# Kernel tuning notes

Measured on AMD Instinct MI355X. Metric: run time of the kernel, lower is better.

Reference implementation:

```python
import jax, jax.numpy as jnp
import numpy as np


def setup_inputs() -> dict:
    key = jax.random.key(0)
    ks = jax.random.split(key, 9)
    b, h, w, c = 32, 64, 64, 256
    s = 0.02  # small init to mimic variance-scaled NIN weights
    return {
        "x": jax.random.normal(ks[0], (b, h, w, c), dtype=jnp.float32),
        "Wq": jax.random.normal(ks[1], (c, c), dtype=jnp.float32) * s,
        "bq": jnp.zeros((c,), dtype=jnp.float32),
        "Wk": jax.random.normal(ks[2], (c, c), dtype=jnp.float32) * s,
        "bk": jnp.zeros((c,), dtype=jnp.float32),
        "Wv": jax.random.normal(ks[3], (c, c), dtype=jnp.float32) * s,
        "bv": jnp.zeros((c,), dtype=jnp.float32),
        "Wo": jax.random.normal(ks[4], (c, c), dtype=jnp.float32) * s,
        "bo": jnp.zeros((c,), dtype=jnp.float32),
    }


def reference(x, Wq, bq, Wk, bk, Wv, bv, Wo, bo):
    # x: [b, h, w, c]. NOTE: in the source, GroupNorm(x) is computed but its
    # output is immediately overwritten (dead code); Q/K/V come from raw x.
    b, h, w, c = x.shape
    cf = jnp.asarray(c, x.dtype)
    Q = jnp.einsum('bhwc,cd->bhwd', x, Wq) + bq
    K = jnp.einsum('bhwc,cd->bhwd', x, Wk) + bk
    V = jnp.einsum('bhwc,cd->bhwd', x, Wv) + bv
    # per-row attention over the W axis: scores [b, h, w, w]
    # double scaling: /(c*sqrt(1/2)) then softmax(./sqrt(c))
    scores = jnp.einsum('bhic,bhjc->bhij', Q, K) / (cf * jnp.sqrt(jnp.asarray(0.5, x.dtype)))
    attn = jax.nn.softmax(scores / jnp.sqrt(cf), axis=-1)
    out = jnp.einsum('bhij,bhjc->bhic', attn, V)
    out = jnp.einsum('bhwc,cd->bhwd', out, Wo) + bo
    return out + x
```

## Files before the change

### kernel.cpp

```cpp
#include <hip/hip_runtime.h>
#include <hip/hip_bf16.h>
#include <stdint.h>


typedef __bf16 bf16x8 __attribute__((ext_vector_type(8)));
typedef __bf16 bf16x4 __attribute__((ext_vector_type(4)));
typedef float f32x4 __attribute__((ext_vector_type(4)));

#define C 256
#define WTOK 64
#define CP 264
#define VP 72
#define PP 72

__device__ float  g_wT[3 * 65536];
__device__ __bf16 g_wqk[65536];
__device__ __bf16 g_wvo[65536];
__device__ float  g_c[256];
__device__ float  g_bvo[256];

__device__ __forceinline__ bf16x8 ld8(const __bf16* p) {
  return *reinterpret_cast<const bf16x8*>(p);
}

__global__ __launch_bounds__(256) void trans_kernel(
    const float* __restrict__ wq, const float* __restrict__ wk,
    const float* __restrict__ wv) {
  __shared__ float tile[32][33];
  const float* src = (blockIdx.z == 0) ? wq : (blockIdx.z == 1) ? wk : wv;
  float* d = &g_wT[0] + (size_t)blockIdx.z * 65536;
  const int tx = threadIdx.x, ty = threadIdx.y;
  const int k0 = blockIdx.x * 32;
  const int m0 = blockIdx.y * 32;
  for (int i = 0; i < 4; ++i)
    tile[ty + 8 * i][tx] = src[(size_t)(k0 + ty + 8 * i) * 256 + m0 + tx];
  __syncthreads();
  for (int i = 0; i < 4; ++i)
    d[(size_t)(m0 + ty + 8 * i) * 256 + k0 + tx] = tile[tx][ty + 8 * i];
}

__global__ __launch_bounds__(256) void fold_kernel(
    const float* __restrict__ wk, const float* __restrict__ wo) {
  const int n = blockIdx.x;
  const int k = threadIdx.x;
  float acc = 0.f;
  if (blockIdx.y == 0) {
    const float* a = &g_wT[0];
    #pragma unroll 8
    for (int m = 0; m < 256; ++m) acc += a[m * 256 + k] * wk[n * 256 + m];
    g_wqk[n * 256 + k] = (__bf16)acc;
  } else {
    const float* a = &g_wT[2 * 65536];
    #pragma unroll 8
    for (int m = 0; m < 256; ++m) acc += a[m * 256 + k] * wo[m * 256 + n];
    g_wvo[n * 256 + k] = (__bf16)acc;
  }
}

__global__ __launch_bounds__(256) void bias_kernel(
    const float* __restrict__ bq, const float* __restrict__ bv,
    const float* __restrict__ bo, const float* __restrict__ wo) {
  const int n = threadIdx.x;
  const float* wkT = &g_wT[65536];
  float c = 0.f, bb = bo[n];
  #pragma unroll 8
  for (int m = 0; m < 256; ++m) c += bq[m] * wkT[m * 256 + n];
  #pragma unroll 8
  for (int k = 0; k < 256; ++k) bb += bv[k] * wo[k * 256 + n];
  g_c[n] = c;
  g_bvo[n] = bb;
}

__global__ __launch_bounds__(256, 2) void attn_fused_kernel(
    const float* __restrict__ x, float* __restrict__ out) {
  __shared__ __align__(16) __bf16 smem[39936];
  __bf16* xs = smem;
  __bf16* ts = smem + 16896;
  __bf16* vt = ts;
  __bf16* ps = smem + 35328;

  const int tid = threadIdx.x;
  const int wv = tid >> 6;
  const int lane = tid & 63;
  const int quad = lane >> 4;
  const int l16 = lane & 15;
  const int bh = blockIdx.x;
  const float* xrow = x + (size_t)bh * (WTOK * C);

  for (int it = 0; it < 16; ++it) {
    const int chunk = tid + it * 256;
    const int row = chunk >> 6;
    const int c4 = (chunk & 63) << 2;
    const float4 v = *reinterpret_cast<const float4*>(xrow + row * 256 + c4);
    bf16x4 b;
    b[0] = (__bf16)v.x; b[1] = (__bf16)v.y; b[2] = (__bf16)v.z; b[3] = (__bf16)v.w;
    *reinterpret_cast<bf16x4*>(xs + row * CP + c4) = b;
  }
  __syncthreads();

  const int nb = wv * 64;
  const int i0 = wv * 16;

  {
    f32x4 D[4][4];
    const f32x4 zero = {0.f, 0.f, 0.f, 0.f};
    for (int m = 0; m < 4; ++m)
      for (int nt = 0; nt < 4; ++nt) D[m][nt] = zero;
    for (int kc = 0; kc < 8; ++kc) {
      const int ko = kc * 32 + quad * 8;
      bf16x8 a[4];
      for (int m = 0; m < 4; ++m) a[m] = ld8(xs + (m * 16 + l16) * CP + ko);
      for (int nt = 0; nt < 4; ++nt) {
        bf16x8 b = ld8(g_wqk + (size_t)(nb + nt * 16 + l16) * 256 + ko);
        for (int m = 0; m < 4; ++m)
          D[m][nt] = __builtin_amdgcn_mfma_f32_16x16x32_bf16(a[m], b, D[m][nt], 0, 0, 0);
      }
    }
    float cs[4];
    for (int nt = 0; nt < 4; ++nt) cs[nt] = g_c[nb + nt * 16 + l16];
    for (int m = 0; m < 4; ++m)
      for (int nt = 0; nt < 4; ++nt)
        for (int r = 0; r < 4; ++r)
          ts[(m * 16 + quad * 4 + r) * CP + nb + nt * 16 + l16] =
              (__bf16)(D[m][nt][r] + cs[nt]);
  }
  __syncthreads();

  f32x4 S[4];
  {
    const f32x4 zero = {0.f, 0.f, 0.f, 0.f};
    for (int nt = 0; nt < 4; ++nt) S[nt] = zero;
    bf16x8 qa[8];
    for (int kc = 0; kc < 8; ++kc)
      qa[kc] = ld8(ts + (i0 + l16) * CP + kc * 32 + quad * 8);
    for (int nt = 0; nt < 4; ++nt)
      for (int kc = 0; kc < 8; ++kc) {
        bf16x8 kb = ld8(xs + (nt * 16 + l16) * CP + kc * 32 + quad * 8);
        S[nt] = __builtin_amdgcn_mfma_f32_16x16x32_bf16(qa[kc], kb, S[nt], 0, 0, 0);
      }
  }

  const float SCALE = 1.0f / (256.0f * 16.0f * 0.70710678118654752f);
  for (int r = 0; r < 4; ++r) {
    float p[4];
    float mx = -1e30f;
    for (int nt = 0; nt < 4; ++nt) {
      p[nt] = S[nt][r] * SCALE;
      mx = fmaxf(mx, p[nt]);
    }
    for (int msk = 1; msk < 16; msk <<= 1) mx = fmaxf(mx, __shfl_xor(mx, msk));
    float sum = 0.f;
    for (int nt = 0; nt < 4; ++nt) {
      p[nt] = __expf(p[nt] - mx);
      sum += p[nt];
    }
    for (int msk = 1; msk < 16; msk <<= 1) sum += __shfl_xor(sum, msk);
    const float invs = 1.0f / sum;
    for (int nt = 0; nt < 4; ++nt)
      ps[(i0 + quad * 4 + r) * PP + nt * 16 + l16] = (__bf16)(p[nt] * invs);
  }
  __syncthreads();

  float xres[64];
  float bvo[16];
  {
    #pragma unroll
    for (int ct = 0; ct < 16; ++ct) bvo[ct] = g_bvo[ct * 16 + l16];
    #pragma unroll
    for (int ct = 0; ct < 16; ++ct)
      #pragma unroll
      for (int r = 0; r < 4; ++r)
        xres[ct * 4 + r] = xrow[(i0 + quad * 4 + r) * 256 + ct * 16 + l16];

    f32x4 D[4][4];
    const f32x4 zero = {0.f, 0.f, 0.f, 0.f};
    for (int m = 0; m < 4; ++m)
      for (int nt = 0; nt < 4; ++nt) D[m][nt] = zero;
    for (int kc = 0; kc < 8; ++kc) {
      const int ko = kc * 32 + quad * 8;
      bf16x8 a[4];
      for (int m = 0; m < 4; ++m) a[m] = ld8(xs + (m * 16 + l16) * CP + ko);
      for (int nt = 0; nt < 4; ++nt) {
        bf16x8 b = ld8(g_wvo + (size_t)(nb + nt * 16 + l16) * 256 + ko);
        for (int m = 0; m < 4; ++m)
          D[m][nt] = __builtin_amdgcn_mfma_f32_16x16x32_bf16(a[m], b, D[m][nt], 0, 0, 0);
      }
    }
    for (int nt = 0; nt < 4; ++nt) {
      const int ch = nb + nt * 16 + l16;
      for (int m = 0; m < 4; ++m) {
        bf16x4 v4;
        for (int r = 0; r < 4; ++r) v4[r] = (__bf16)D[m][nt][r];
        *reinterpret_cast<bf16x4*>(vt + ch * VP + m * 16 + quad * 4) = v4;
      }
    }
  }
  __syncthreads();

  {
    f32x4 Y[16];
    const f32x4 zero = {0.f, 0.f, 0.f, 0.f};
    for (int ct = 0; ct < 16; ++ct) Y[ct] = zero;
    bf16x8 pa[2];
    for (int kc = 0; kc < 2; ++kc)
      pa[kc] = ld8(ps + (i0 + l16) * PP + kc * 32 + quad * 8);
    #pragma unroll
    for (int ct = 0; ct < 16; ++ct) {
      #pragma unroll
      for (int kc = 0; kc < 2; ++kc) {
        bf16x8 vb = ld8(vt + (ct * 16 + l16) * VP + kc * 32 + quad * 8);
        Y[ct] = __builtin_amdgcn_mfma_f32_16x16x32_bf16(pa[kc], vb, Y[ct], 0, 0, 0);
      }
    }
    #pragma unroll
    for (int ct = 0; ct < 16; ++ct) {
      const int ch = ct * 16 + l16;
      #pragma unroll
      for (int r = 0; r < 4; ++r) {
        const int tok = i0 + quad * 4 + r;
        out[((size_t)bh * WTOK + tok) * C + ch] = Y[ct][r] + bvo[ct] + xres[ct * 4 + r];
      }
    }
  }
}

extern "C" void kernel_launch(void* const* d_in, const int* in_sizes, int n_in,
                              void* d_out, int out_size, void* d_ws, size_t ws_size,
                              hipStream_t stream) {
  (void)in_sizes; (void)n_in; (void)out_size; (void)d_ws; (void)ws_size;
  const float* x  = (const float*)d_in[0];
  const float* Wq = (const float*)d_in[1];
  const float* bq = (const float*)d_in[2];
  const float* Wk = (const float*)d_in[3];
  const float* Wv = (const float*)d_in[5];
  const float* bv = (const float*)d_in[6];
  const float* Wo = (const float*)d_in[7];
  const float* bo = (const float*)d_in[8];
  float* out = (float*)d_out;

  hipLaunchKernelGGL(trans_kernel, dim3(8, 8, 3), dim3(32, 8, 1), 0, stream, Wq, Wk, Wv);
  hipLaunchKernelGGL(fold_kernel, dim3(256, 2, 1), dim3(256), 0, stream, Wk, Wo);
  hipLaunchKernelGGL(bias_kernel, dim3(1), dim3(256), 0, stream, bq, bv, bo, Wo);
  hipLaunchKernelGGL(attn_fused_kernel, dim3(2048), dim3(256), 0, stream, x, out);
}
```

Before: 358.5 us.

## Transpose MFMA operand roles for vectorized stores and fold bias kernel into fold

Swaps the A/B operands of the MFMAs in the QK-projection, score and PV stages so each lane's accumulator holds four consecutive channels or keys. The Q^T store, the softmax probabilities and the final output can then be written as packed bf16x4 and float4 vectors, with the residual and bias loaded as float4. The softmax reduction needs only two cross-lane shuffles instead of four per row. Separately, the bias computation is merged into fold_kernel and the Wk transpose is dropped, removing one launch and some preprocessing; the residual is now read after the MFMAs instead of being held in registers beforehand.

```diff
diff --git a/kernel.cpp b/kernel.cpp
--- a/kernel.cpp
+++ b/kernel.cpp
@@ -13,7 +13,7 @@
 #define VP 72
 #define PP 72
 
-__device__ float  g_wT[3 * 65536];
+__device__ float  g_wT[2 * 65536];
 __device__ __bf16 g_wqk[65536];
 __device__ __bf16 g_wvo[65536];
 __device__ float  g_c[256];
@@ -24,10 +24,9 @@
 }
 
 __global__ __launch_bounds__(256) void trans_kernel(
-    const float* __restrict__ wq, const float* __restrict__ wk,
-    const float* __restrict__ wv) {
+    const float* __restrict__ wq, const float* __restrict__ wv) {
   __shared__ float tile[32][33];
-  const float* src = (blockIdx.z == 0) ? wq : (blockIdx.z == 1) ? wk : wv;
+  const float* src = (blockIdx.z == 0) ? wq : wv;
   float* d = &g_wT[0] + (size_t)blockIdx.z * 65536;
   const int tx = threadIdx.x, ty = threadIdx.y;
   const int k0 = blockIdx.x * 32;
@@ -40,35 +39,34 @@
 }
 
 __global__ __launch_bounds__(256) void fold_kernel(
-    const float* __restrict__ wk, const float* __restrict__ wo) {
+    const float* __restrict__ wk, const float* __restrict__ wo,
+    const float* __restrict__ bq, const float* __restrict__ bv,
+    const float* __restrict__ bo) {
   const int n = blockIdx.x;
   const int k = threadIdx.x;
-  float acc = 0.f;
   if (blockIdx.y == 0) {
     const float* a = &g_wT[0];
+    float acc = 0.f, c = 0.f;
     #pragma unroll 8
-    for (int m = 0; m < 256; ++m) acc += a[m * 256 + k] * wk[n * 256 + m];
+    for (int m = 0; m < 256; ++m) {
+      const float w = wk[n * 256 + m];
+      acc += a[m * 256 + k] * w;
+      c += bq[m] * w;
+    }
     g_wqk[n * 256 + k] = (__bf16)acc;
+    if (k == 0) g_c[n] = c;
   } else {
-    const float* a = &g_wT[2 * 65536];
+    const float* a = &g_wT[65536];
+    float acc = 0.f, bb = 0.f;
     #pragma unroll 8
-    for (int m = 0; m < 256; ++m) acc += a[m * 256 + k] * wo[m * 256 + n];
+    for (int m = 0; m < 256; ++m) {
+      const float w = wo[m * 256 + n];
+      acc += a[m * 256 + k] * w;
+      bb += bv[m] * w;
+    }
     g_wvo[n * 256 + k] = (__bf16)acc;
-  }
-}
-
-__global__ __launch_bounds__(256) void bias_kernel(
-    const float* __restrict__ bq, const float* __restrict__ bv,
-    const float* __restrict__ bo, const float* __restrict__ wo) {
-  const int n = threadIdx.x;
-  const float* wkT = &g_wT[65536];
-  float c = 0.f, bb = bo[n];
-  #pragma unroll 8
-  for (int m = 0; m < 256; ++m) c += bq[m] * wkT[m * 256 + n];
-  #pragma unroll 8
-  for (int k = 0; k < 256; ++k) bb += bv[k] * wo[k * 256 + n];
-  g_c[n] = c;
-  g_bvo[n] = bb;
+    if (k == 0) g_bvo[n] = bb + bo[n];
+  }
 }
 
 __global__ __launch_bounds__(256, 2) void attn_fused_kernel(
@@ -105,24 +103,30 @@
     f32x4 D[4][4];
     const f32x4 zero = {0.f, 0.f, 0.f, 0.f};
     for (int m = 0; m < 4; ++m)
-      for (int nt = 0; nt < 4; ++nt) D[m][nt] = zero;
+      for (int t = 0; t < 4; ++t) D[m][t] = zero;
     for (int kc = 0; kc < 8; ++kc) {
       const int ko = kc * 32 + quad * 8;
       bf16x8 a[4];
-      for (int m = 0; m < 4; ++m) a[m] = ld8(xs + (m * 16 + l16) * CP + ko);
-      for (int nt = 0; nt < 4; ++nt) {
-        bf16x8 b = ld8(g_wqk + (size_t)(nb + nt * 16 + l16) * 256 + ko);
+      for (int m = 0; m < 4; ++m)
+        a[m] = ld8(g_wqk + (size_t)(nb + m * 16 + l16) * 256 + ko);
+      for (int t = 0; t < 4; ++t) {
+        bf16x8 b = ld8(xs + (t * 16 + l16) * CP + ko);
         for (int m = 0; m < 4; ++m)
-          D[m][nt] = __builtin_amdgcn_mfma_f32_16x16x32_bf16(a[m], b, D[m][nt], 0, 0, 0);
-      }
-    }
-    float cs[4];
-    for (int nt = 0; nt < 4; ++nt) cs[nt] = g_c[nb + nt * 16 + l16];
-    for (int m = 0; m < 4; ++m)
-      for (int nt = 0; nt < 4; ++nt)
-        for (int r = 0; r < 4; ++r)
-          ts[(m * 16 + quad * 4 + r) * CP + nb + nt * 16 + l16] =
-              (__bf16)(D[m][nt][r] + cs[nt]);
+          D[m][t] = __builtin_amdgcn_mfma_f32_16x16x32_bf16(a[m], b, D[m][t], 0, 0, 0);
+      }
+    }
+    float4 cs[4];
+    for (int m = 0; m < 4; ++m)
+      cs[m] = *reinterpret_cast<const float4*>(g_c + nb + m * 16 + quad * 4);
+    for (int m = 0; m < 4; ++m)
+      for (int t = 0; t < 4; ++t) {
+        bf16x4 v4;
+        v4[0] = (__bf16)(D[m][t][0] + cs[m].x);
+        v4[1] = (__bf16)(D[m][t][1] + cs[m].y);
+        v4[2] = (__bf16)(D[m][t][2] + cs[m].z);
+        v4[3] = (__bf16)(D[m][t][3] + cs[m].w);
+        *reinterpret_cast<bf16x4*>(ts + (t * 16 + l16) * CP + nb + m * 16 + quad * 4) = v4;
+      }
   }
   __syncthreads();
 
@@ -130,48 +134,44 @@
   {
     const f32x4 zero = {0.f, 0.f, 0.f, 0.f};
     for (int nt = 0; nt < 4; ++nt) S[nt] = zero;
-    bf16x8 qa[8];
+    bf16x8 qb[8];
     for (int kc = 0; kc < 8; ++kc)
-      qa[kc] = ld8(ts + (i0 + l16) * CP + kc * 32 + quad * 8);
+      qb[kc] = ld8(ts + (i0 + l16) * CP + kc * 32 + quad * 8);
     for (int nt = 0; nt < 4; ++nt)
       for (int kc = 0; kc < 8; ++kc) {
-        bf16x8 kb = ld8(xs + (nt * 16 + l16) * CP + kc * 32 + quad * 8);
-        S[nt] = __builtin_amdgcn_mfma_f32_16x16x32_bf16(qa[kc], kb, S[nt], 0, 0, 0);
+        bf16x8 ka = ld8(xs + (nt * 16 + l16) * CP + kc * 32 + quad * 8);
+        S[nt] = __builtin_amdgcn_mfma_f32_16x16x32_bf16(ka, qb[kc], S[nt], 0, 0, 0);
       }
   }
 
   const float SCALE = 1.0f / (256.0f * 16.0f * 0.70710678118654752f);
-  for (int r = 0; r < 4; ++r) {
-    float p[4];
+  {
+    float p[16];
     float mx = -1e30f;
+    for (int nt = 0; nt < 4; ++nt)
+      for (int r = 0; r < 4; ++r) {
+        p[nt * 4 + r] = S[nt][r] * SCALE;
+        mx = fmaxf(mx, p[nt * 4 + r]);
+      }
+    mx = fmaxf(mx, __shfl_xor(mx, 16));
+    mx = fmaxf(mx, __shfl_xor(mx, 32));
+    float sum = 0.f;
+    for (int i = 0; i < 16; ++i) {
+      p[i] = __expf(p[i] - mx);
+      sum += p[i];
+    }
+    sum += __shfl_xor(sum, 16);
+    sum += __shfl_xor(sum, 32);
+    const float invs = 1.0f / sum;
     for (int nt = 0; nt < 4; ++nt) {
-      p[nt] = S[nt][r] * SCALE;
-      mx = fmaxf(mx, p[nt]);
-    }
-    for (int msk = 1; msk < 16; msk <<= 1) mx = fmaxf(mx, __shfl_xor(mx, msk));
-    float sum = 0.f;
-    for (int nt = 0; nt < 4; ++nt) {
-      p[nt] = __expf(p[nt] - mx);
-      sum += p[nt];
-    }
-    for (int msk = 1; msk < 16; msk <<= 1) sum += __shfl_xor(sum, msk);
-    const float invs = 1.0f / sum;
-    for (int nt = 0; nt < 4; ++nt)
-      ps[(i0 + quad * 4 + r) * PP + nt * 16 + l16] = (__bf16)(p[nt] * invs);
-  }
-  __syncthreads();
-
-  float xres[64];
-  float bvo[16];
-  {
-    #pragma unroll
-    for (int ct = 0; ct < 16; ++ct) bvo[ct] = g_bvo[ct * 16 + l16];
-    #pragma unroll
-    for (int ct = 0; ct < 16; ++ct)
-      #pragma unroll
-      for (int r = 0; r < 4; ++r)
-        xres[ct * 4 + r] = xrow[(i0 + quad * 4 + r) * 256 + ct * 16 + l16];
-
+      bf16x4 v4;
+      for (int r = 0; r < 4; ++r) v4[r] = (__bf16)(p[nt * 4 + r] * invs);
+      *reinterpret_cast<bf16x4*>(ps + (i0 + l16) * PP + nt * 16 + quad * 4) = v4;
+    }
+  }
+  __syncthreads();
+
+  {
     f32x4 D[4][4];
     const f32x4 zero = {0.f, 0.f, 0.f, 0.f};
     for (int m = 0; m < 4; ++m)
@@ -201,25 +201,31 @@
     f32x4 Y[16];
     const f32x4 zero = {0.f, 0.f, 0.f, 0.f};
     for (int ct = 0; ct < 16; ++ct) Y[ct] = zero;
-    bf16x8 pa[2];
+    bf16x8 pb[2];
     for (int kc = 0; kc < 2; ++kc)
-      pa[kc] = ld8(ps + (i0 + l16) * PP + kc * 32 + quad * 8);
+      pb[kc] = ld8(ps + (i0 + l16) * PP + kc * 32 + quad * 8);
     #pragma unroll
     for (int ct = 0; ct < 16; ++ct) {
       #pragma unroll
       for (int kc = 0; kc < 2; ++kc) {
-        bf16x8 vb = ld8(vt + (ct * 16 + l16) * VP + kc * 32 + quad * 8);
-        Y[ct] = __builtin_amdgcn_mfma_f32_16x16x32_bf16(pa[kc], vb, Y[ct], 0, 0, 0);
-      }
-    }
+        bf16x8 va = ld8(vt + (ct * 16 + l16) * VP + kc * 32 + quad * 8);
+        Y[ct] = __builtin_amdgcn_mfma_f32_16x16x32_bf16(va, pb[kc], Y[ct], 0, 0, 0);
+      }
+    }
+    const int q = i0 + l16;
+    const float* xr = xrow + q * 256;
+    float* outr = out + ((size_t)bh * WTOK + q) * C;
     #pragma unroll
     for (int ct = 0; ct < 16; ++ct) {
-      const int ch = ct * 16 + l16;
-      #pragma unroll
-      for (int r = 0; r < 4; ++r) {
-        const int tok = i0 + quad * 4 + r;
-        out[((size_t)bh * WTOK + tok) * C + ch] = Y[ct][r] + bvo[ct] + xres[ct * 4 + r];
-      }
+      const int ch = ct * 16 + quad * 4;
+      const float4 bv4 = *reinterpret_cast<const float4*>(g_bvo + ch);
+      const float4 xres = *reinterpret_cast<const float4*>(xr + ch);
+      float4 o;
+      o.x = Y[ct][0] + bv4.x + xres.x;
+      o.y = Y[ct][1] + bv4.y + xres.y;
+      o.z = Y[ct][2] + bv4.z + xres.z;
+      o.w = Y[ct][3] + bv4.w + xres.w;
+      *reinterpret_cast<float4*>(outr + ch) = o;
     }
   }
 }
@@ -238,8 +244,7 @@
   const float* bo = (const float*)d_in[8];
   float* out = (float*)d_out;
 
-  hipLaunchKernelGGL(trans_kernel, dim3(8, 8, 3), dim3(32, 8, 1), 0, stream, Wq, Wk, Wv);
-  hipLaunchKernelGGL(fold_kernel, dim3(256, 2, 1), dim3(256), 0, stream, Wk, Wo);
-  hipLaunchKernelGGL(bias_kernel, dim3(1), dim3(256), 0, stream, bq, bv, bo, Wo);
+  hipLaunchKernelGGL(trans_kernel, dim3(8, 8, 2), dim3(32, 8, 1), 0, stream, Wq, Wv);
+  hipLaunchKernelGGL(fold_kernel, dim3(256, 2, 1), dim3(256), 0, stream, Wk, Wo, bq, bv, bo);
   hipLaunchKernelGGL(attn_fused_kernel, dim3(2048), dim3(256), 0, stream, x, out);
 }
```

After: 361.2 us. Within noise of the previous version (+0.8%).
